# Performance work log

Measured on AMD Instinct MI355X. Metric: run time of the kernel, lower is better.

Reference implementation:

```python
import jax, jax.numpy as jnp
import numpy as np

N = 200000
M0, M1, M2 = 128, 64, 32          # input/output multiplicities for l=0,1,2
H0, H1, H2 = 384, 192, 96         # mlp_mid multiplicities for l=0,1,2
G = H1 + H2                        # number of gate scalars (one per gated channel)
INV_M0 = 1.0 / float(np.sqrt(M0)); INV_M1 = 1.0 / float(np.sqrt(M1)); INV_M2 = 1.0 / float(np.sqrt(M2))
INV_H0 = 1.0 / float(np.sqrt(H0)); INV_H1 = 1.0 / float(np.sqrt(H1)); INV_H2 = 1.0 / float(np.sqrt(H2))


def setup_inputs() -> dict:
    key = jax.random.key(0)
    ks = jax.random.split(key, 12)
    D = M0 + 3 * M1 + 5 * M2  # 480, e3nn layout: [128x0e | 64x1e (64,3) | 32x2e (32,5)]
    node_input = jax.random.normal(ks[0], (N, D), dtype=jnp.float32)
    node_attr = jnp.ones((N, 1), dtype=jnp.float32)  # '1x0e' constant attribute
    # fctp_1 (FCTP + SwishGate): paths l x 0e -> l; extra 0e gate scalars from 0e x 0e
    W0s = jax.random.normal(ks[1], (M0, H0), dtype=jnp.float32)
    b_s = jax.random.normal(ks[2], (H0,), dtype=jnp.float32) * 0.1
    W0g = jax.random.normal(ks[3], (M0, G), dtype=jnp.float32)
    b_g = jax.random.normal(ks[4], (G,), dtype=jnp.float32) * 0.1
    W1 = jax.random.normal(ks[5], (M1, H1), dtype=jnp.float32)
    W2 = jax.random.normal(ks[6], (M2, H2), dtype=jnp.float32)
    # fctp_2 (FCTP, bias on 0e output only)
    V0 = jax.random.normal(ks[7], (H0, M0), dtype=jnp.float32)
    b_o = jax.random.normal(ks[8], (M0,), dtype=jnp.float32) * 0.1
    V1 = jax.random.normal(ks[9], (H1, M1), dtype=jnp.float32)
    V2 = jax.random.normal(ks[10], (H2, M2), dtype=jnp.float32)
    return dict(node_input=node_input, node_attr=node_attr, W0s=W0s, b_s=b_s,
                W0g=W0g, b_g=b_g, W1=W1, W2=W2, V0=V0, b_o=b_o, V1=V1, V2=V2)


def reference(node_input, node_attr, W0s, b_s, W0g, b_g, W1, W2, V0, b_o, V1, V2):
    n = node_input.shape[0]
    x0 = node_input[:, :M0]                                   # [N,128]
    x1 = node_input[:, M0:M0 + 3 * M1].reshape(n, M1, 3)      # [N,64,3]
    x2 = node_input[:, M0 + 3 * M1:].reshape(n, M2, 5)        # [N,32,5]
    y = node_attr                                             # [N,1] scalar attr
    y3 = y[:, :, None]
    # --- fctp_1 + SwishGate (rescale: divide each path by sqrt(fan_in)) ---
    s = jax.nn.silu((x0 @ W0s) * (y * INV_M0) + b_s)          # [N,384] mid scalars
    g = jax.nn.sigmoid((x0 @ W0g) * (y * INV_M0) + b_g)       # [N,288] gates
    v1 = jnp.einsum('num,uw->nwm', x1, W1) * (y3 * INV_M1) * g[:, :H1, None]   # [N,192,3]
    v2 = jnp.einsum('num,uw->nwm', x2, W2) * (y3 * INV_M2) * g[:, H1:, None]   # [N,96,5]
    # --- fctp_2 (bias on scalar output only) ---
    o0 = (s @ V0) * (y * INV_H0) + b_o                        # [N,128]
    o1 = jnp.einsum('num,uw->nwm', v1, V1) * (y3 * INV_H1)    # [N,64,3]
    o2 = jnp.einsum('num,uw->nwm', v2, V2) * (y3 * INV_H2)    # [N,32,5]
    return jnp.concatenate([o0, o1.reshape(n, -1), o2.reshape(n, -1)], axis=-1)  # [N,480]
```

## Files before the change

### kernel.cpp

```cpp
#include <hip/hip_runtime.h>


typedef __attribute__((ext_vector_type(8))) short short8;
typedef __attribute__((ext_vector_type(4))) float f32x4;

#define INV_M0f 0.08838834764831845f
#define INV_M1f 0.125f
#define INV_M2f 0.17677669529663687f
#define INV_H0f 0.05103103630798288f
#define INV_H1f 0.07216878364870323f
#define INV_H2f 0.10206207261596577f

#define OFF_W0T 0
#define OFF_W1T 86016
#define OFF_W2T 98304
#define OFF_V0T 101376
#define OFF_V1T 150528
#define OFF_V2T 162816
#define WP_TOTAL 165888

__device__ __forceinline__ short f2bf_rne(float f) {
    union { float f; unsigned u; } v; v.f = f;
    unsigned r = v.u + 0x7FFFu + ((v.u >> 16) & 1u);
    return (short)(r >> 16);
}
__device__ __forceinline__ short f2bf_fast(float f) {
    unsigned r;
    asm("v_cvt_pk_bf16_f32 %0, %1, %1" : "=v"(r) : "v"(f));
    return (short)r;
}
__device__ __forceinline__ float bf2f(short s) {
    union { unsigned u; float f; } v; v.u = ((unsigned)(unsigned short)s) << 16;
    return v.f;
}

__global__ void prep_weights(const float* __restrict__ W0s, const float* __restrict__ W0g,
                             const float* __restrict__ W1,  const float* __restrict__ W2,
                             const float* __restrict__ V0,  const float* __restrict__ V1,
                             const float* __restrict__ V2,  short* __restrict__ ws)
{
    int i = blockIdx.x * 256 + threadIdx.x;
    if (i < 86016) {
        int j = i >> 7, k = i & 127;
        float v = (j < 384) ? W0s[k * 384 + j] : W0g[k * 288 + (j - 384)];
        ws[i] = f2bf_rne(v * INV_M0f);
    } else if (i < 98304) {
        int e = i - 86016; int w = e >> 6, u = e & 63;
        ws[i] = f2bf_rne(W1[u * 192 + w] * INV_M1f);
    } else if (i < 101376) {
        int e = i - 98304; int w = e >> 5, u = e & 31;
        ws[i] = f2bf_rne(W2[u * 96 + w] * INV_M2f);
    } else if (i < 150528) {
        int e = i - 101376; int j = e / 384, w = e % 384;
        ws[i] = f2bf_rne(V0[w * 128 + j] * INV_H0f);
    } else if (i < 162816) {
        int e = i - 150528; int j = e / 192, w = e % 192;
        ws[i] = f2bf_rne(V1[w * 64 + j] * INV_H1f);
    } else if (i < WP_TOTAL) {
        int e = i - 162816; int j = e / 96, w = e % 96;
        ws[i] = f2bf_rne(V2[w * 32 + j] * INV_H2f);
    }
}

#define X0_STRIDE 136
#define SB_OFF 4352
#define SB_STRIDE 392
#define GB_OFF 16896
#define GB_STRIDE 296
#define UB_OFF 6912
#define UB_STRIDE 200
#define LDS_SHORTS 26368

#define MFMA(a, b, c) __builtin_amdgcn_mfma_f32_16x16x32_bf16((a), (b), (c), 0, 0, 0)

__global__ __launch_bounds__(512, 4) void ffn_main(
    const float* __restrict__ X, const float* __restrict__ Y,
    const float* __restrict__ bs, const float* __restrict__ bg, const float* __restrict__ bo,
    const short* __restrict__ WP, float* __restrict__ out)
{
    __shared__ short lds[LDS_SHORTS];
    short* x0s  = lds;
    short* sbuf = lds + SB_OFF;
    short* gbuf = lds + GB_OFF;
    short* x1T  = lds;
    short* x2T  = lds;
    short* ubuf = lds + UB_OFF;

    const int tid  = threadIdx.x;
    const int wid  = tid >> 6;
    const int lane = tid & 63;
    const int m    = lane & 15;
    const int bq   = lane >> 4;
    const int n0   = blockIdx.x * 32;

    short8 w0c[4];
    float bias_c;
    {
        const short* w = WP + OFF_W0T + (wid * 16 + m) * 128 + bq * 8;
        #pragma unroll
        for (int k = 0; k < 4; ++k) w0c[k] = *(const short8*)(w + k * 32);
        bias_c = bs[wid * 16 + m];
    }

    {
        const int node = tid >> 4, c16 = tid & 15;
        const float* xp = X + (size_t)(n0 + node) * 480 + c16 * 8;
        float4 f0 = *(const float4*)xp;
        float4 f1 = *(const float4*)(xp + 4);
        short8 a;
        a[0]=f2bf_fast(f0.x); a[1]=f2bf_fast(f0.y); a[2]=f2bf_fast(f0.z); a[3]=f2bf_fast(f0.w);
        a[4]=f2bf_fast(f1.x); a[5]=f2bf_fast(f1.y); a[6]=f2bf_fast(f1.z); a[7]=f2bf_fast(f1.w);
        *(short8*)(x0s + node * X0_STRIDE + c16 * 8) = a;
    }

    float yv[2][4];
    #pragma unroll
    for (int t = 0; t < 2; ++t)
        #pragma unroll
        for (int r = 0; r < 4; ++r)
            yv[t][r] = Y[n0 + t * 16 + bq * 4 + r];

    __syncthreads();

    short8 a0[2][4];
    #pragma unroll
    for (int t = 0; t < 2; ++t)
        #pragma unroll
        for (int k = 0; k < 4; ++k)
            a0[t][k] = *(const short8*)(x0s + (t * 16 + m) * X0_STRIDE + k * 32 + bq * 8);

    #pragma unroll 1
    for (int i = 0; i < 6; ++i) {
        const int jt = wid + i * 8;
        if (jt >= 42) break;
        const int jn = jt + 8;
        short8 w0n[4];
        float bias_n = 0.f;
        if (jn < 42) {
            const short* w = WP + OFF_W0T + (jn * 16 + m) * 128 + bq * 8;
            #pragma unroll
            for (int k = 0; k < 4; ++k) w0n[k] = *(const short8*)(w + k * 32);
            bias_n = (jn < 24) ? bs[jn * 16 + m] : bg[(jn - 24) * 16 + m];
        }
        f32x4 acc0 = {0.f,0.f,0.f,0.f}, acc1 = {0.f,0.f,0.f,0.f};
        #pragma unroll
        for (int k = 0; k < 4; ++k) {
            acc0 = MFMA(a0[0][k], w0c[k], acc0);
            acc1 = MFMA(a0[1][k], w0c[k], acc1);
        }
        if (jt < 24) {
            #pragma unroll
            for (int t = 0; t < 2; ++t) {
                f32x4 acc = t ? acc1 : acc0;
                #pragma unroll
                for (int r = 0; r < 4; ++r) {
                    float val = fmaf(acc[r], yv[t][r], bias_c);
                    float e   = __expf(-val);
                    float sv  = val * __builtin_amdgcn_rcpf(1.f + e);
                    sbuf[(t * 16 + bq * 4 + r) * SB_STRIDE + jt * 16 + m] = f2bf_fast(sv);
                }
            }
        } else {
            #pragma unroll
            for (int t = 0; t < 2; ++t) {
                f32x4 acc = t ? acc1 : acc0;
                #pragma unroll
                for (int r = 0; r < 4; ++r) {
                    float val = fmaf(acc[r], yv[t][r], bias_c);
                    float e   = __expf(-val);
                    float sg  = __builtin_amdgcn_rcpf(1.f + e);
                    gbuf[(t * 16 + bq * 4 + r) * GB_STRIDE + (jt - 24) * 16 + m] = f2bf_fast(sg);
                }
            }
        }
        #pragma unroll
        for (int k = 0; k < 4; ++k) w0c[k] = w0n[k];
        bias_c = bias_n;
    }

    short8 v0f[12];
    {
        const short* v = WP + OFF_V0T + (wid * 16 + m) * 384 + bq * 8;
        #pragma unroll
        for (int k = 0; k < 12; ++k) v0f[k] = *(const short8*)(v + k * 32);
    }
    const float bo_r = bo[wid * 16 + m];
    __syncthreads();

    {
        f32x4 accD0 = {0.f,0.f,0.f,0.f}, accD1 = {0.f,0.f,0.f,0.f};
        #pragma unroll
        for (int k = 0; k < 12; ++k) {
            short8 sa0 = *(const short8*)(sbuf + m * SB_STRIDE + k * 32 + bq * 8);
            short8 sa1 = *(const short8*)(sbuf + (16 + m) * SB_STRIDE + k * 32 + bq * 8);
            accD0 = MFMA(sa0, v0f[k], accD0);
            accD1 = MFMA(sa1, v0f[k], accD1);
        }
        #pragma unroll
        for (int t = 0; t < 2; ++t) {
            f32x4 acc = t ? accD1 : accD0;
            #pragma unroll
            for (int r = 0; r < 4; ++r)
                out[(size_t)(n0 + t * 16 + bq * 4 + r) * 480 + wid * 16 + m] =
                    fmaf(acc[r], yv[t][r], bo_r);
        }
    }

    short8 w1f[2][2];
    #pragma unroll
    for (int jj = 0; jj < 2; ++jj) {
        const int jt = wid + jj * 8;
        if (jt < 12) {
            const short* w = WP + OFF_W1T + (jt * 16 + m) * 64 + bq * 8;
            w1f[jj][0] = *(const short8*)(w);
            w1f[jj][1] = *(const short8*)(w + 32);
        }
    }
    short8 v1f[6];
    if (wid >= 4) {
        const short* v = WP + OFF_V1T + ((wid - 4) * 16 + m) * 192 + bq * 8;
        #pragma unroll
        for (int k = 0; k < 6; ++k) v1f[k] = *(const short8*)(v + k * 32);
    }
    __syncthreads();

    {
        const int node = tid >> 4, c16 = tid & 15;
        const float* xp = X + (size_t)(n0 + node) * 480 + 128 + c16 * 12;
        float4 fa = *(const float4*)xp;
        float4 fb = *(const float4*)(xp + 4);
        float4 fc = *(const float4*)(xp + 8);
        float vals[12] = {fa.x,fa.y,fa.z,fa.w, fb.x,fb.y,fb.z,fb.w, fc.x,fc.y,fc.z,fc.w};
        #pragma unroll
        for (int c = 0; c < 12; ++c) {
            const int u   = c16 * 4 + c / 3;
            const int mmv = c % 3;
            x1T[mmv * 2304 + node * 72 + u] = f2bf_fast(vals[c]);
        }
    }
    __syncthreads();

    float o1a[3][2][4];
    #pragma unroll
    for (int mm = 0; mm < 3; ++mm) {
        #pragma unroll
        for (int jj = 0; jj < 2; ++jj) {
            const int jt = wid + jj * 8;
            if (jt < 12) {
                f32x4 accA = {0.f,0.f,0.f,0.f}, accB = {0.f,0.f,0.f,0.f};
                short8 a00 = *(const short8*)(x1T + mm * 2304 + m * 72 + bq * 8);
                short8 a01 = *(const short8*)(x1T + mm * 2304 + m * 72 + 32 + bq * 8);
                short8 a10 = *(const short8*)(x1T + mm * 2304 + (16 + m) * 72 + bq * 8);
                short8 a11 = *(const short8*)(x1T + mm * 2304 + (16 + m) * 72 + 32 + bq * 8);
                accA = MFMA(a00, w1f[jj][0], accA);
                accA = MFMA(a01, w1f[jj][1], accA);
                accB = MFMA(a10, w1f[jj][0], accB);
                accB = MFMA(a11, w1f[jj][1], accB);
                #pragma unroll
                for (int t = 0; t < 2; ++t) {
                    f32x4 acc = t ? accB : accA;
                    #pragma unroll
                    for (int r = 0; r < 4; ++r) {
                        const int node = t * 16 + bq * 4 + r;
                        float gv = bf2f(gbuf[node * GB_STRIDE + jt * 16 + m]);
                        ubuf[node * UB_STRIDE + jt * 16 + m] =
                            f2bf_fast(acc[r] * yv[t][r] * gv);
                    }
                }
            }
        }
        __syncthreads();
        if (wid >= 4) {
            f32x4 accA = {0.f,0.f,0.f,0.f}, accB = {0.f,0.f,0.f,0.f};
            #pragma unroll
            for (int k = 0; k < 6; ++k) {
                short8 au0 = *(const short8*)(ubuf + m * UB_STRIDE + k * 32 + bq * 8);
                short8 au1 = *(const short8*)(ubuf + (16 + m) * UB_STRIDE + k * 32 + bq * 8);
                accA = MFMA(au0, v1f[k], accA);
                accB = MFMA(au1, v1f[k], accB);
            }
            #pragma unroll
            for (int t = 0; t < 2; ++t) {
                f32x4 acc = t ? accB : accA;
                #pragma unroll
                for (int r = 0; r < 4; ++r)
                    o1a[mm][t][r] = acc[r] * yv[t][r];
            }
        }
        __syncthreads();
    }
    if (wid >= 4) {
        const int jc = (wid - 4) * 16 + m;
        #pragma unroll
        for (int t = 0; t < 2; ++t)
            #pragma unroll
            for (int r = 0; r < 4; ++r) {
                float* p = out + (size_t)(n0 + t * 16 + bq * 4 + r) * 480 + 128 + jc * 3;
                p[0] = o1a[0][t][r]; p[1] = o1a[1][t][r]; p[2] = o1a[2][t][r];
            }
    }

    short8 w2f;
    if (wid < 6)
        w2f = *(const short8*)(WP + OFF_W2T + (wid * 16 + m) * 32 + bq * 8);
    short8 v2f[3];
    if (wid >= 6) {
        const short* v = WP + OFF_V2T + ((wid - 6) * 16 + m) * 96 + bq * 8;
        #pragma unroll
        for (int k = 0; k < 3; ++k) v2f[k] = *(const short8*)(v + k * 32);
    }

    {
        const int node = tid >> 4, c16 = tid & 15;
        const float* xp = X + (size_t)(n0 + node) * 480 + 320 + c16 * 10;
        float vals[10];
        #pragma unroll
        for (int p = 0; p < 5; ++p) {
            float2 f = *(const float2*)(xp + p * 2);
            vals[p * 2] = f.x; vals[p * 2 + 1] = f.y;
        }
        #pragma unroll
        for (int c = 0; c < 10; ++c) {
            const int u   = c16 * 2 + c / 5;
            const int mmv = c % 5;
            x2T[mmv * 1280 + node * 40 + u] = f2bf_fast(vals[c]);
        }
    }
    __syncthreads();

    float o2a[5][2][4];
    #pragma unroll
    for (int mm = 0; mm < 5; ++mm) {
        if (wid < 6) {
            f32x4 accA = {0.f,0.f,0.f,0.f}, accB = {0.f,0.f,0.f,0.f};
            short8 a20 = *(const short8*)(x2T + mm * 1280 + m * 40 + bq * 8);
            short8 a21 = *(const short8*)(x2T + mm * 1280 + (16 + m) * 40 + bq * 8);
            accA = MFMA(a20, w2f, accA);
            accB = MFMA(a21, w2f, accB);
            #pragma unroll
            for (int t = 0; t < 2; ++t) {
                f32x4 acc = t ? accB : accA;
                #pragma unroll
                for (int r = 0; r < 4; ++r) {
                    const int node = t * 16 + bq * 4 + r;
                    float gv = bf2f(gbuf[node * GB_STRIDE + 192 + wid * 16 + m]);
                    ubuf[node * UB_STRIDE + wid * 16 + m] =
                        f2bf_fast(acc[r] * yv[t][r] * gv);
                }
            }
        }
        __syncthreads();
        if (wid >= 6) {
            f32x4 accA = {0.f,0.f,0.f,0.f}, accB = {0.f,0.f,0.f,0.f};
            #pragma unroll
            for (int k = 0; k < 3; ++k) {
                short8 au0 = *(const short8*)(ubuf + m * UB_STRIDE + k * 32 + bq * 8);
                short8 au1 = *(const short8*)(ubuf + (16 + m) * UB_STRIDE + k * 32 + bq * 8);
                accA = MFMA(au0, v2f[k], accA);
                accB = MFMA(au1, v2f[k], accB);
            }
            #pragma unroll
            for (int t = 0; t < 2; ++t) {
                f32x4 acc = t ? accB : accA;
                #pragma unroll
                for (int r = 0; r < 4; ++r)
                    o2a[mm][t][r] = acc[r] * yv[t][r];
            }
        }
        if (mm < 4) __syncthreads();
    }
    if (wid >= 6) {
        const int jc = (wid - 6) * 16 + m;
        #pragma unroll
        for (int t = 0; t < 2; ++t)
            #pragma unroll
            for (int r = 0; r < 4; ++r) {
                float* p = out + (size_t)(n0 + t * 16 + bq * 4 + r) * 480 + 320 + jc * 5;
                p[0] = o2a[0][t][r]; p[1] = o2a[1][t][r]; p[2] = o2a[2][t][r];
                p[3] = o2a[3][t][r]; p[4] = o2a[4][t][r];
            }
    }
}

extern "C" void kernel_launch(void* const* d_in, const int* in_sizes, int n_in,
                              void* d_out, int out_size, void* d_ws, size_t ws_size,
                              hipStream_t stream)
{
    const float* X   = (const float*)d_in[0];
    const float* Y   = (const float*)d_in[1];
    const float* W0s = (const float*)d_in[2];
    const float* bs  = (const float*)d_in[3];
    const float* W0g = (const float*)d_in[4];
    const float* bg  = (const float*)d_in[5];
    const float* W1  = (const float*)d_in[6];
    const float* W2  = (const float*)d_in[7];
    const float* V0  = (const float*)d_in[8];
    const float* bo  = (const float*)d_in[9];
    const float* V1  = (const float*)d_in[10];
    const float* V2  = (const float*)d_in[11];
    short* WP  = (short*)d_ws;
    float* out = (float*)d_out;

    const int n = in_sizes[0] / 480;
    const int tiles = n / 32;

    prep_weights<<<dim3((WP_TOTAL + 255) / 256), dim3(256), 0, stream>>>(
        W0s, W0g, W1, W2, V0, V1, V2, WP);
    ffn_main<<<dim3(tiles), dim3(512), 0, stream>>>(X, Y, bs, bg, bo, WP, out);
}
```

Baseline: 334.1 us.

## Batch all m-components of l=1/l=2 paths into single GEMMs with balanced wave split

Instead of looping over the 3 (l=1) and 5 (l=2) spherical components with a barrier per component and only some waves active, the l=1 and l=2 stages now treat components as extra rows: all 96 (or 160) rows are processed at once. The output tiles are spread evenly across all 8 waves, which cuts the number of __syncthreads calls and the idle waves. The x2 global load is also overlapped with the l=1 second-stage GEMM. In exchange LDS use rises from about 52 KB to about 71 KB per block, which may limit how many blocks fit on a CU, and W1/W2 fragments are now reloaded from global memory for each tile.

```diff
diff --git a/kernel.cpp b/kernel.cpp
--- a/kernel.cpp
+++ b/kernel.cpp
@@ -65,11 +65,13 @@
 #define X0_STRIDE 136
 #define SB_OFF 4352
 #define SB_STRIDE 392
-#define GB_OFF 16896
+#define GB_OFF 26112
 #define GB_STRIDE 296
-#define UB_OFF 6912
-#define UB_STRIDE 200
-#define LDS_SHORTS 26368
+#define UB1_OFF 6912
+#define UB1_STRIDE 200
+#define UB2_OFF 6400
+#define UB2_STRIDE 104
+#define LDS_SHORTS 35584
 
 #define MFMA(a, b, c) __builtin_amdgcn_mfma_f32_16x16x32_bf16((a), (b), (c), 0, 0, 0)
 
@@ -79,12 +81,13 @@
     const short* __restrict__ WP, float* __restrict__ out)
 {
     __shared__ short lds[LDS_SHORTS];
-    short* x0s  = lds;
-    short* sbuf = lds + SB_OFF;
-    short* gbuf = lds + GB_OFF;
-    short* x1T  = lds;
-    short* x2T  = lds;
-    short* ubuf = lds + UB_OFF;
+    short* x0s   = lds;
+    short* sbuf  = lds + SB_OFF;
+    short* gbuf  = lds + GB_OFF;
+    short* x1T   = lds;
+    short* x2T   = lds;
+    short* ubuf1 = lds + UB1_OFF;
+    short* ubuf2 = lds + UB2_OFF;
 
     const int tid  = threadIdx.x;
     const int wid  = tid >> 6;
@@ -206,19 +209,10 @@
         }
     }
 
-    short8 w1f[2][2];
-    #pragma unroll
-    for (int jj = 0; jj < 2; ++jj) {
-        const int jt = wid + jj * 8;
-        if (jt < 12) {
-            const short* w = WP + OFF_W1T + (jt * 16 + m) * 64 + bq * 8;
-            w1f[jj][0] = *(const short8*)(w);
-            w1f[jj][1] = *(const short8*)(w + 32);
-        }
-    }
+    const int ct1 = wid & 3, p1 = wid >> 2;
     short8 v1f[6];
-    if (wid >= 4) {
-        const short* v = WP + OFF_V1T + ((wid - 4) * 16 + m) * 192 + bq * 8;
+    {
+        const short* v = WP + OFF_V1T + (ct1 * 16 + m) * 192 + bq * 8;
         #pragma unroll
         for (int k = 0; k < 6; ++k) v1f[k] = *(const short8*)(v + k * 32);
     }
@@ -235,150 +229,140 @@
         for (int c = 0; c < 12; ++c) {
             const int u   = c16 * 4 + c / 3;
             const int mmv = c % 3;
-            x1T[mmv * 2304 + node * 72 + u] = f2bf_fast(vals[c]);
-        }
-    }
-    __syncthreads();
-
-    float o1a[3][2][4];
-    #pragma unroll
-    for (int mm = 0; mm < 3; ++mm) {
-        #pragma unroll
-        for (int jj = 0; jj < 2; ++jj) {
-            const int jt = wid + jj * 8;
-            if (jt < 12) {
-                f32x4 accA = {0.f,0.f,0.f,0.f}, accB = {0.f,0.f,0.f,0.f};
-                short8 a00 = *(const short8*)(x1T + mm * 2304 + m * 72 + bq * 8);
-                short8 a01 = *(const short8*)(x1T + mm * 2304 + m * 72 + 32 + bq * 8);
-                short8 a10 = *(const short8*)(x1T + mm * 2304 + (16 + m) * 72 + bq * 8);
-                short8 a11 = *(const short8*)(x1T + mm * 2304 + (16 + m) * 72 + 32 + bq * 8);
-                accA = MFMA(a00, w1f[jj][0], accA);
-                accA = MFMA(a01, w1f[jj][1], accA);
-                accB = MFMA(a10, w1f[jj][0], accB);
-                accB = MFMA(a11, w1f[jj][1], accB);
-                #pragma unroll
-                for (int t = 0; t < 2; ++t) {
-                    f32x4 acc = t ? accB : accA;
-                    #pragma unroll
-                    for (int r = 0; r < 4; ++r) {
-                        const int node = t * 16 + bq * 4 + r;
-                        float gv = bf2f(gbuf[node * GB_STRIDE + jt * 16 + m]);
-                        ubuf[node * UB_STRIDE + jt * 16 + m] =
-                            f2bf_fast(acc[r] * yv[t][r] * gv);
-                    }
-                }
-            }
-        }
-        __syncthreads();
-        if (wid >= 4) {
-            f32x4 accA = {0.f,0.f,0.f,0.f}, accB = {0.f,0.f,0.f,0.f};
+            x1T[(mmv * 32 + node) * 72 + u] = f2bf_fast(vals[c]);
+        }
+    }
+    __syncthreads();
+
+    {
+        f32x4 accs[9];
+        #pragma unroll
+        for (int ii = 0; ii < 9; ++ii) {
+            const unsigned idx = (unsigned)(wid * 9 + ii);
+            const int ct = idx / 6u, rt = idx % 6u;
+            const short* wb = WP + OFF_W1T + (ct * 16 + m) * 64 + bq * 8;
+            short8 b0 = *(const short8*)(wb);
+            short8 b1 = *(const short8*)(wb + 32);
+            short8 a00 = *(const short8*)(x1T + (rt * 16 + m) * 72 + bq * 8);
+            short8 a01 = *(const short8*)(x1T + (rt * 16 + m) * 72 + 32 + bq * 8);
+            f32x4 acc = {0.f,0.f,0.f,0.f};
+            acc = MFMA(a00, b0, acc);
+            acc = MFMA(a01, b1, acc);
+            accs[ii] = acc;
+        }
+        #pragma unroll
+        for (int ii = 0; ii < 9; ++ii) {
+            const unsigned idx = (unsigned)(wid * 9 + ii);
+            const int ct = idx / 6u, rt = idx % 6u;
+            const int w = ct * 16 + m;
+            #pragma unroll
+            for (int r = 0; r < 4; ++r) {
+                const int node = (rt & 1) * 16 + bq * 4 + r;
+                float gv = bf2f(gbuf[node * GB_STRIDE + w]);
+                ubuf1[(rt * 16 + bq * 4 + r) * UB1_STRIDE + w] =
+                    f2bf_fast(accs[ii][r] * yv[rt & 1][r] * gv);
+            }
+        }
+    }
+    __syncthreads();
+
+    {
+        const int node2 = tid >> 4, c16 = tid & 15;
+        const float* xp2 = X + (size_t)(n0 + node2) * 480 + 320 + c16 * 10;
+        float vals[10];
+        #pragma unroll
+        for (int p = 0; p < 5; ++p) {
+            float2 f = *(const float2*)(xp2 + p * 2);
+            vals[p * 2] = f.x; vals[p * 2 + 1] = f.y;
+        }
+        f32x4 o1f[3];
+        #pragma unroll
+        for (int q = 0; q < 3; ++q) {
+            const int rt = q * 2 + p1;
+            f32x4 acc = {0.f,0.f,0.f,0.f};
             #pragma unroll
             for (int k = 0; k < 6; ++k) {
-                short8 au0 = *(const short8*)(ubuf + m * UB_STRIDE + k * 32 + bq * 8);
-                short8 au1 = *(const short8*)(ubuf + (16 + m) * UB_STRIDE + k * 32 + bq * 8);
-                accA = MFMA(au0, v1f[k], accA);
-                accB = MFMA(au1, v1f[k], accB);
-            }
-            #pragma unroll
-            for (int t = 0; t < 2; ++t) {
-                f32x4 acc = t ? accB : accA;
-                #pragma unroll
-                for (int r = 0; r < 4; ++r)
-                    o1a[mm][t][r] = acc[r] * yv[t][r];
-            }
-        }
-        __syncthreads();
-    }
-    if (wid >= 4) {
-        const int jc = (wid - 4) * 16 + m;
-        #pragma unroll
-        for (int t = 0; t < 2; ++t)
-            #pragma unroll
-            for (int r = 0; r < 4; ++r) {
-                float* p = out + (size_t)(n0 + t * 16 + bq * 4 + r) * 480 + 128 + jc * 3;
-                p[0] = o1a[0][t][r]; p[1] = o1a[1][t][r]; p[2] = o1a[2][t][r];
-            }
-    }
-
-    short8 w2f;
-    if (wid < 6)
-        w2f = *(const short8*)(WP + OFF_W2T + (wid * 16 + m) * 32 + bq * 8);
-    short8 v2f[3];
-    if (wid >= 6) {
-        const short* v = WP + OFF_V2T + ((wid - 6) * 16 + m) * 96 + bq * 8;
-        #pragma unroll
-        for (int k = 0; k < 3; ++k) v2f[k] = *(const short8*)(v + k * 32);
-    }
-
-    {
-        const int node = tid >> 4, c16 = tid & 15;
-        const float* xp = X + (size_t)(n0 + node) * 480 + 320 + c16 * 10;
-        float vals[10];
-        #pragma unroll
-        for (int p = 0; p < 5; ++p) {
-            float2 f = *(const float2*)(xp + p * 2);
-            vals[p * 2] = f.x; vals[p * 2 + 1] = f.y;
+                short8 a = *(const short8*)(ubuf1 + (rt * 16 + m) * UB1_STRIDE + k * 32 + bq * 8);
+                acc = MFMA(a, v1f[k], acc);
+            }
+            o1f[q] = acc;
+        }
+        #pragma unroll
+        for (int r = 0; r < 4; ++r) {
+            const float yy = yv[p1][r];
+            float* pp = out + (size_t)(n0 + p1 * 16 + bq * 4 + r) * 480 + 128 + (ct1 * 16 + m) * 3;
+            pp[0] = o1f[0][r] * yy; pp[1] = o1f[1][r] * yy; pp[2] = o1f[2][r] * yy;
         }
         #pragma unroll
         for (int c = 0; c < 10; ++c) {
             const int u   = c16 * 2 + c / 5;
             const int mmv = c % 5;
-            x2T[mmv * 1280 + node * 40 + u] = f2bf_fast(vals[c]);
-        }
-    }
-    __syncthreads();
-
-    float o2a[5][2][4];
-    #pragma unroll
-    for (int mm = 0; mm < 5; ++mm) {
-        if (wid < 6) {
-            f32x4 accA = {0.f,0.f,0.f,0.f}, accB = {0.f,0.f,0.f,0.f};
-            short8 a20 = *(const short8*)(x2T + mm * 1280 + m * 40 + bq * 8);
-            short8 a21 = *(const short8*)(x2T + mm * 1280 + (16 + m) * 40 + bq * 8);
-            accA = MFMA(a20, w2f, accA);
-            accB = MFMA(a21, w2f, accB);
-            #pragma unroll
-            for (int t = 0; t < 2; ++t) {
-                f32x4 acc = t ? accB : accA;
+            x2T[(mmv * 32 + node2) * 40 + u] = f2bf_fast(vals[c]);
+        }
+    }
+
+    short8 v2f[3];
+    if (wid < 4) {
+        const short* v = WP + OFF_V2T + ((wid & 1) * 16 + m) * 96 + bq * 8;
+        #pragma unroll
+        for (int k = 0; k < 3; ++k) v2f[k] = *(const short8*)(v + k * 32);
+    }
+    __syncthreads();
+
+    {
+        const int ntile = (wid < 4) ? 8 : 7;
+        const int base  = (wid < 4) ? wid * 8 : 32 + (wid - 4) * 7;
+        f32x4 accs[8];
+        #pragma unroll
+        for (int ii = 0; ii < 8; ++ii) {
+            if (ii < ntile) {
+                const unsigned idx = (unsigned)(base + ii);
+                const int rt = idx / 6u, ct = idx % 6u;
+                short8 b = *(const short8*)(WP + OFF_W2T + (ct * 16 + m) * 32 + bq * 8);
+                short8 a = *(const short8*)(x2T + (rt * 16 + m) * 40 + bq * 8);
+                f32x4 z = {0.f,0.f,0.f,0.f};
+                accs[ii] = MFMA(a, b, z);
+            }
+        }
+        #pragma unroll
+        for (int ii = 0; ii < 8; ++ii) {
+            if (ii < ntile) {
+                const unsigned idx = (unsigned)(base + ii);
+                const int rt = idx / 6u, ct = idx % 6u;
+                const int w = ct * 16 + m;
                 #pragma unroll
                 for (int r = 0; r < 4; ++r) {
-                    const int node = t * 16 + bq * 4 + r;
-                    float gv = bf2f(gbuf[node * GB_STRIDE + 192 + wid * 16 + m]);
-                    ubuf[node * UB_STRIDE + wid * 16 + m] =
-                        f2bf_fast(acc[r] * yv[t][r] * gv);
+                    const int node = (rt & 1) * 16 + bq * 4 + r;
+                    float gv = bf2f(gbuf[node * GB_STRIDE + 192 + w]);
+                    ubuf2[(rt * 16 + bq * 4 + r) * UB2_STRIDE + w] =
+                        f2bf_fast(accs[ii][r] * yv[rt & 1][r] * gv);
                 }
             }
         }
-        __syncthreads();
-        if (wid >= 6) {
-            f32x4 accA = {0.f,0.f,0.f,0.f}, accB = {0.f,0.f,0.f,0.f};
+    }
+    __syncthreads();
+
+    if (wid < 4) {
+        const int ct2 = wid & 1, p2 = wid >> 1;
+        f32x4 o2f[5];
+        #pragma unroll
+        for (int q = 0; q < 5; ++q) {
+            const int rt = q * 2 + p2;
+            f32x4 acc = {0.f,0.f,0.f,0.f};
             #pragma unroll
             for (int k = 0; k < 3; ++k) {
-                short8 au0 = *(const short8*)(ubuf + m * UB_STRIDE + k * 32 + bq * 8);
-                short8 au1 = *(const short8*)(ubuf + (16 + m) * UB_STRIDE + k * 32 + bq * 8);
-                accA = MFMA(au0, v2f[k], accA);
-                accB = MFMA(au1, v2f[k], accB);
-            }
-            #pragma unroll
-            for (int t = 0; t < 2; ++t) {
-                f32x4 acc = t ? accB : accA;
-                #pragma unroll
-                for (int r = 0; r < 4; ++r)
-                    o2a[mm][t][r] = acc[r] * yv[t][r];
-            }
-        }
-        if (mm < 4) __syncthreads();
-    }
-    if (wid >= 6) {
-        const int jc = (wid - 6) * 16 + m;
-        #pragma unroll
-        for (int t = 0; t < 2; ++t)
-            #pragma unroll
-            for (int r = 0; r < 4; ++r) {
-                float* p = out + (size_t)(n0 + t * 16 + bq * 4 + r) * 480 + 320 + jc * 5;
-                p[0] = o2a[0][t][r]; p[1] = o2a[1][t][r]; p[2] = o2a[2][t][r];
-                p[3] = o2a[3][t][r]; p[4] = o2a[4][t][r];
-            }
+                short8 a = *(const short8*)(ubuf2 + (rt * 16 + m) * UB2_STRIDE + k * 32 + bq * 8);
+                acc = MFMA(a, v2f[k], acc);
+            }
+            o2f[q] = acc;
+        }
+        #pragma unroll
+        for (int r = 0; r < 4; ++r) {
+            const float yy = yv[p2][r];
+            float* pp = out + (size_t)(n0 + p2 * 16 + bq * 4 + r) * 480 + 320 + (ct2 * 16 + m) * 5;
+            pp[0] = o2f[0][r] * yy; pp[1] = o2f[1][r] * yy; pp[2] = o2f[2][r] * yy;
+            pp[3] = o2f[3][r] * yy; pp[4] = o2f[4][r] * yy;
+        }
     }
 }
 
```

Measured after the change: 461.2 us. 38.0% more time.
